# Performance work log

Measured on AMD Instinct MI355X. Metric: run time of the kernel, lower is better.

## Reference

```python
import jax, jax.numpy as jnp
import numpy as np

N = 16384      # nodes
E = 262144     # static edges (avg degree 16)
D = 128        # node embedding dim
DE = 64        # edge embedding dim
H = 256        # MLP hidden dim
K = 16         # dynamic kNN


def _w(key, shape, scale=0.05):
    return jax.random.normal(key, shape, dtype=jnp.float32) * scale


def setup_inputs() -> dict:
    key = jax.random.key(0)
    ks = jax.random.split(key, 32)
    inp = {
        "x": jax.random.normal(ks[0], (N, D), dtype=jnp.float32),
        "edge_attr": jax.random.normal(ks[1], (E, DE), dtype=jnp.float32),
        # static conv msg MLPs (3 layers stacked): in 192 -> 256 -> 128
        "sW1": _w(ks[2], (3, D + DE, H)), "sb1": jnp.zeros((3, H), jnp.float32),
        "sW2": _w(ks[3], (3, H, D)),      "sb2": jnp.zeros((3, D), jnp.float32),
        # static conv update MLPs: 128 -> 256 -> 128
        "uW1": _w(ks[4], (3, D, H)), "ub1": jnp.zeros((3, H), jnp.float32),
        "uW2": _w(ks[5], (3, H, D)), "ub2": jnp.zeros((3, D), jnp.float32),
        # edge refiners between static convs: 64 -> 64
        "rW": _w(ks[6], (2, DE, DE)), "rb": jnp.zeros((2, DE), jnp.float32),
        # dynamic conv msg MLPs (2 layers stacked): in 256 -> 256 -> 128
        "dW1": _w(ks[7], (2, 2 * D, H)), "db1": jnp.zeros((2, H), jnp.float32),
        "dW2": _w(ks[8], (2, H, D)),     "db2": jnp.zeros((2, D), jnp.float32),
        # dynamic conv update MLPs: 128 -> 256 -> 128
        "dUW1": _w(ks[9], (2, D, H)),  "dUb1": jnp.zeros((2, H), jnp.float32),
        "dUW2": _w(ks[10], (2, H, D)), "dUb2": jnp.zeros((2, D), jnp.float32),
        # fuse MLP: 256 -> 256 -> 128
        "fW1": _w(ks[11], (2 * D, H)), "fb1": jnp.zeros((H,), jnp.float32),
        "fW2": _w(ks[12], (H, D)),     "fb2": jnp.zeros((D,), jnp.float32),
        "edge_index": jax.random.randint(ks[13], (2, E), 0, N, dtype=jnp.int64),
        "k": K,
    }
    return inp


def _mlp2(h, W1, b1, W2, b2):
    # SequentialBlock: Linear -> ReLU -> Linear -> ReLU
    return jax.nn.relu(jax.nn.relu(h @ W1 + b1) @ W2 + b2)


def _knn_edges(x, k):
    # squared euclidean distances, [N, N]; self included (dist 0 -> self loops)
    sq = jnp.sum(x * x, axis=1)
    d = sq[:, None] - 2.0 * (x @ x.T) + sq[None, :]
    _, nbr = jax.lax.top_k(-d, k)                  # [N, k] sources per target
    src = nbr.reshape(-1)
    dst = jnp.repeat(jnp.arange(x.shape[0]), k)
    return src, dst


def reference(x, edge_attr, sW1, sb1, sW2, sb2, uW1, ub1, uW2, ub2, rW, rb,
              dW1, db1, dW2, db2, dUW1, dUb1, dUW2, dUb2,
              fW1, fb1, fW2, fb2, edge_index, k):
    n = x.shape[0]
    src, dst = edge_index[0], edge_index[1]  # PyG: row=source(j), col=target(i)

    # ---- static branch: 3 StaticConv ('vanilla') with edge refiners ----
    xs, ea = x, edge_attr
    for i in range(3):
        msg_in = jnp.concatenate([ea, xs[src] - xs[dst]], axis=1)  # [E, DE+D]
        m = _mlp2(msg_in, sW1[i], sb1[i], sW2[i], sb2[i])
        agg = jax.ops.segment_sum(m, dst, num_segments=n)
        xs = _mlp2(agg, uW1[i], ub1[i], uW2[i], ub2[i])
        if i < 2:
            ea = jax.nn.relu(ea @ rW[i] + rb[i])  # EdgeEmbedRefiner

    # ---- dynamic branch: 2 DynamicGonv ('vanilla', kNN on current emb) ----
    xd = x
    for i in range(2):
        dsrc, ddst = _knn_edges(xd, k)
        xi = xd[ddst]
        xj = xd[dsrc]
        m = _mlp2(jnp.concatenate([xi, xj - xi], axis=1), dW1[i], db1[i], dW2[i], db2[i])
        agg = jax.ops.segment_sum(m, ddst, num_segments=n)
        xd = _mlp2(agg, dUW1[i], dUb1[i], dUW2[i], dUb2[i])

    # ---- fuse ----
    h = jnp.concatenate([xs, xd], axis=1)  # [N, 2D]
    return _mlp2(h, fW1, fb1, fW2, fb2)
```

## Files before the change

### kernel.cpp

```cpp
#include <hip/hip_runtime.h>

#define Nn 16384
#define Ee 262144
#define Dd 128
#define DEe 64
#define Hh 256
#define KK 16
#define NSPLIT 16
#define TT 128
#define STILE 128
#define SWEEP (Nn / NSPLIT)
#define PXS 136
#define PDD 68
#define MCAND 32
#define BDEPTH 8
#define LDEPTH 8

typedef __attribute__((ext_vector_type(8))) short short8;
typedef __attribute__((ext_vector_type(4))) float floatx4;

__device__ __forceinline__ ushort f2bf(float f) {
  uint u = __float_as_uint(f);
  u += 0x7fffu + ((u >> 16) & 1u);
  return (ushort)(u >> 16);
}
__device__ __forceinline__ float bf2f(ushort h) { return __uint_as_float(((uint)h) << 16); }
__device__ __forceinline__ void cvt_hilo(float4 v, uint2* hi, uint2* lo) {
  ushort h0 = f2bf(v.x), h1 = f2bf(v.y), h2 = f2bf(v.z), h3 = f2bf(v.w);
  ushort l0 = f2bf(v.x - bf2f(h0)), l1 = f2bf(v.y - bf2f(h1));
  ushort l2 = f2bf(v.z - bf2f(h2)), l3 = f2bf(v.w - bf2f(h3));
  hi->x = (uint)h0 | ((uint)h1 << 16); hi->y = (uint)h2 | ((uint)h3 << 16);
  lo->x = (uint)l0 | ((uint)l1 << 16); lo->y = (uint)l2 | ((uint)l3 << 16);
}
__device__ __forceinline__ uint4 pk8(float4 a, float4 b) {
  uint4 o;
  o.x = (uint)f2bf(a.x) | ((uint)f2bf(a.y) << 16);
  o.y = (uint)f2bf(a.z) | ((uint)f2bf(a.w) << 16);
  o.z = (uint)f2bf(b.x) | ((uint)f2bf(b.y) << 16);
  o.w = (uint)f2bf(b.z) | ((uint)f2bf(b.w) << 16);
  return o;
}

__device__ __forceinline__ int ld_src(const int* ei, int e, int mode) {
  return mode ? ei[e] : ei[2 * e];
}
__device__ __forceinline__ int ld_dst(const int* ei, int e, int mode) {
  return mode ? ei[Ee + e] : ei[2 * Ee + 2 * e];
}

__global__ void k_detect(const int* __restrict__ ei, int* __restrict__ flag) {
  if (blockIdx.x == 0 && threadIdx.x == 0) {
    int any = 0;
    for (int i = 0; i < 64; ++i) any |= ei[2 * i + 1];
    *flag = (any != 0) ? 1 : 0;
  }
}

__global__ void k_hist(const int* __restrict__ ei, const int* __restrict__ mode_p,
                       int* __restrict__ hist) {
  int e = blockIdx.x * 256 + threadIdx.x;
  int mode = *mode_p;
  atomicAdd(&hist[ld_dst(ei, e, mode)], 1);
}

__global__ void k_scan(const int* __restrict__ hist, int* __restrict__ cursor) {
  __shared__ int part[256];
  __shared__ int partx[256];
  int t = threadIdx.x;
  int base = t * (Nn / 256);
  int s = 0;
  for (int i = 0; i < Nn / 256; ++i) s += hist[base + i];
  part[t] = s;
  __syncthreads();
  if (t == 0) {
    int run = 0;
    for (int i = 0; i < 256; ++i) { partx[i] = run; run += part[i]; }
  }
  __syncthreads();
  int run = partx[t];
  for (int i = 0; i < Nn / 256; ++i) { int v = hist[base + i]; cursor[base + i] = run; run += v; }
}

__global__ void k_scatter(const int* __restrict__ ei, const int* __restrict__ mode_p,
                          int* __restrict__ cursor, int* __restrict__ perm,
                          int* __restrict__ dstS) {
  int e = blockIdx.x * 256 + threadIdx.x;
  int mode = *mode_p;
  int d = ld_dst(ei, e, mode);
  int pos = atomicAdd(&cursor[d], 1);
  perm[pos] = e;
  dstS[pos] = d;
}

__global__ void k_sq(const float* __restrict__ x, float* __restrict__ sq,
                     ushort* __restrict__ xbf) {
  int n = blockIdx.x * 256 + threadIdx.x;
  const float4* p = (const float4*)(x + (size_t)n * Dd);
  uint4* ob = (uint4*)(xbf + (size_t)n * Dd);
  float acc = 0.f;
#pragma unroll
  for (int i = 0; i < Dd / 8; ++i) {
    float4 v = p[2 * i];
    acc += v.x * v.x + v.y * v.y + v.z * v.z + v.w * v.w;
    float4 w = p[2 * i + 1];
    acc += w.x * w.x + w.y * w.y + w.z * w.z + w.w * w.w;
    ob[i] = pk8(v, w);
  }
  sq[n] = acc;
}

__global__ void k_repack(const float* __restrict__ sW1, const float* __restrict__ sW2,
                         const float* __restrict__ dW1, const float* __restrict__ dW2,
                         uint4* __restrict__ out) {
  int gid = blockIdx.x * 256 + threadIdx.x;
  const float* W; int K, N, u, obase;
  if (gid < 36864) {
    int i = gid / 12288; u = gid - i * 12288;
    W = sW1 + (size_t)i * 49152; K = 192; N = 256; obase = i * 12288;
  } else if (gid < 61440) {
    int g = gid - 36864; int i = g / 8192; u = g - i * 8192;
    W = sW2 + (size_t)i * 32768; K = 256; N = 128; obase = 36864 + i * 8192;
  } else if (gid < 94208) {
    int g = gid - 61440; int i = g / 16384; u = g - i * 16384;
    W = dW1 + (size_t)i * 65536; K = 256; N = 256; obase = 61440 + i * 16384;
  } else if (gid < 110592) {
    int g = gid - 94208; int i = g / 8192; u = g - i * 8192;
    W = dW2 + (size_t)i * 32768; K = 256; N = 128; obase = 94208 + i * 8192;
  } else return;
  int lane = u & 63;
  int t = u >> 6;
  int ksteps = K / 16;
  int kstep = t % ksteps, ntile = t / ksteps;
  int R = K / 32;
  bool lo = kstep >= R;
  int k0 = (lo ? kstep - R : kstep) * 32 + (lane >> 4) * 8;
  int n = ntile * 16 + (lane & 15);
  ushort v[8];
#pragma unroll
  for (int j = 0; j < 8; ++j) {
    float w = W[(size_t)(k0 + j) * N + n];
    ushort h = f2bf(w);
    v[j] = lo ? f2bf(w - bf2f(h)) : h;
  }
  uint4 o;
  o.x = (uint)v[0] | ((uint)v[1] << 16);
  o.y = (uint)v[2] | ((uint)v[3] << 16);
  o.z = (uint)v[4] | ((uint)v[5] << 16);
  o.w = (uint)v[6] | ((uint)v[7] << 16);
  out[obase + u] = o;
}

template <int RK, int NT>
__device__ __forceinline__ void mfma3(const ushort* aB, int pitch, const uint4* __restrict__ Wp,
                                      int lane, floatx4 C[2][NT]) {
  int q = lane >> 4, m0 = lane & 15;
  short8 ahc[RK][2];
#pragma unroll
  for (int hm = 0; hm < 2; ++hm)
#pragma unroll
    for (int nt = 0; nt < NT; ++nt)
#pragma unroll
      for (int rr = 0; rr < 4; ++rr) C[hm][nt][rr] = 0.f;
#pragma unroll
  for (int s = 0; s < RK; ++s) {
    short8 ah0 = *(const short8*)(aB + m0 * pitch + s * 32 + q * 8);
    short8 ah1 = *(const short8*)(aB + (m0 + 16) * pitch + s * 32 + q * 8);
    short8 al0 = *(const short8*)(aB + m0 * pitch + (RK + s) * 32 + q * 8);
    short8 al1 = *(const short8*)(aB + (m0 + 16) * pitch + (RK + s) * 32 + q * 8);
    ahc[s][0] = ah0;
    ahc[s][1] = ah1;
#pragma unroll
    for (int nt = 0; nt < NT; ++nt) {
      uint4 bw = Wp[(nt * 2 * RK + s) * 64 + lane];
      short8 b = *(short8*)&bw;
      C[0][nt] = __builtin_amdgcn_mfma_f32_16x16x32_bf16(ah0, b, C[0][nt], 0, 0, 0);
      C[1][nt] = __builtin_amdgcn_mfma_f32_16x16x32_bf16(ah1, b, C[1][nt], 0, 0, 0);
      C[0][nt] = __builtin_amdgcn_mfma_f32_16x16x32_bf16(al0, b, C[0][nt], 0, 0, 0);
      C[1][nt] = __builtin_amdgcn_mfma_f32_16x16x32_bf16(al1, b, C[1][nt], 0, 0, 0);
    }
  }
#pragma unroll
  for (int s = 0; s < RK; ++s) {
#pragma unroll
    for (int nt = 0; nt < NT; ++nt) {
      uint4 bw = Wp[(nt * 2 * RK + RK + s) * 64 + lane];
      short8 b = *(short8*)&bw;
      C[0][nt] = __builtin_amdgcn_mfma_f32_16x16x32_bf16(ahc[s][0], b, C[0][nt], 0, 0, 0);
      C[1][nt] = __builtin_amdgcn_mfma_f32_16x16x32_bf16(ahc[s][1], b, C[1][nt], 0, 0, 0);
    }
  }
}

__global__ __launch_bounds__(256, 3) void k_knn_part(const ushort* __restrict__ xbf,
                                                     const float* __restrict__ sq,
                                                     float* __restrict__ part_d,
                                                     int* __restrict__ part_i) {
  __shared__ __align__(16) ushort smXS[128 * PXS];
  __shared__ float sqs_l[STILE];
  __shared__ ushort smBuf[BDEPTH * 256];
  float* dtile = (float*)smXS;
  float* mbD = (float*)smXS;
  int* mbI = ((int*)smXS) + 2048;
  int tid = threadIdx.x;
  int wave = tid >> 6, lane = tid & 63;
  int quad = lane >> 4, n15 = lane & 15;
  int tileT = blockIdx.x >> 4;
  int split = blockIdx.x & 15;
  int tb = tileT * TT;
  int tg = tid >> 1, sl = tid & 1;

  float sqi8[8];
#pragma unroll
  for (int mt = 0; mt < 2; ++mt)
#pragma unroll
    for (int rr = 0; rr < 4; ++rr)
      sqi8[mt * 4 + rr] = sq[tb + wave * 32 + mt * 16 + quad * 4 + rr];

  short8 afr[2][4];
#pragma unroll
  for (int mt = 0; mt < 2; ++mt) {
    int row = tb + wave * 32 + mt * 16 + n15;
#pragma unroll
    for (int ks = 0; ks < 4; ++ks)
      afr[mt][ks] = *(const short8*)&xbf[(size_t)row * Dd + ks * 32 + quad * 8];
  }

  float bd[LDEPTH];
  int bi[LDEPTH];
#pragma unroll
  for (int p2 = 0; p2 < LDEPTH; ++p2) { bd[p2] = 3.0e38f; bi[p2] = 0x7fffffff; }
  int bcnt = 0;

  auto ins = [&](float d, int gidx) {
#pragma unroll
    for (int p = LDEPTH - 1; p >= 1; --p) {
      bool shift = d < bd[p - 1];
      bool here = (!shift) && (d < bd[p]);
      float nb = shift ? bd[p - 1] : (here ? d : bd[p]);
      int ni = shift ? bi[p - 1] : (here ? gidx : bi[p]);
      bd[p] = nb;
      bi[p] = ni;
    }
    if (d < bd[0]) { bd[0] = d; bi[0] = gidx; }
  };

#pragma unroll 1
  for (int st = 0; st < SWEEP / STILE; ++st) {
    int sb = split * SWEEP + st * STILE;
    __syncthreads();
    {
      int row = tid & 127, kh = (tid >> 7) * 64;
      int swz = ((row >> 3) & 7) << 3;
      const ushort* src = &xbf[(size_t)(sb + row) * Dd + kh];
#pragma unroll
      for (int g = 0; g < 8; ++g) {
        int k0 = kh + g * 8;
        *(uint4*)&smXS[row * PXS + (k0 ^ swz)] = *(const uint4*)&src[g * 8];
      }
      if (tid < STILE) sqs_l[tid] = sq[sb + tid];
    }
    __syncthreads();
    floatx4 C[2][8];
#pragma unroll
    for (int mt = 0; mt < 2; ++mt)
#pragma unroll
      for (int nt = 0; nt < 8; ++nt)
#pragma unroll
        for (int rr = 0; rr < 4; ++rr) C[mt][nt][rr] = 0.f;
#pragma unroll
    for (int nt = 0; nt < 8; ++nt) {
      int s = nt * 16 + n15;
      int swz = ((s >> 3) & 7) << 3;
#pragma unroll
      for (int ks = 0; ks < 4; ++ks) {
        int k0 = ks * 32 + quad * 8;
        short8 bfr = *(const short8*)&smXS[s * PXS + (k0 ^ swz)];
        C[0][nt] = __builtin_amdgcn_mfma_f32_16x16x32_bf16(afr[0][ks], bfr, C[0][nt], 0, 0, 0);
        C[1][nt] = __builtin_amdgcn_mfma_f32_16x16x32_bf16(afr[1][ks], bfr, C[1][nt], 0, 0, 0);
      }
    }
    float sc[8];
#pragma unroll
    for (int nt = 0; nt < 8; ++nt) sc[nt] = sqs_l[nt * 16 + n15];
    __syncthreads();
#pragma unroll
    for (int h = 0; h < 2; ++h) {
      if (h) __syncthreads();
#pragma unroll
      for (int mt = 0; mt < 2; ++mt)
#pragma unroll
        for (int nt = 0; nt < 4; ++nt)
#pragma unroll
          for (int rr = 0; rr < 4; ++rr) {
            int row = wave * 32 + mt * 16 + quad * 4 + rr;
            int col = nt * 16 + n15;
            float d = fmaf(-2.f, C[mt][nt + 4 * h][rr], sqi8[mt * 4 + rr]) + sc[nt + 4 * h];
            dtile[row * PDD + col] = d;
          }
      __syncthreads();
      const float* drow = &dtile[tg * PDD];
      int cbase = sl * 32;
#pragma unroll 1
      for (int j = 0; j < 8; ++j) {
        float4 v = *(const float4*)&drow[cbase + j * 4];
        float mn = fminf(fminf(v.x, v.y), fminf(v.z, v.w));
        if (mn < bd[LDEPTH - 1]) {
          float dv0 = v.x, dv1 = v.y, dv2 = v.z, dv3 = v.w;
#pragma unroll
          for (int e = 0; e < 4; ++e) {
            float d = (e == 0) ? dv0 : (e == 1) ? dv1 : (e == 2) ? dv2 : dv3;
            if (d < bd[LDEPTH - 1]) {
              int col = cbase + j * 4 + e;
              if (bcnt < BDEPTH) {
                smBuf[bcnt * 256 + tid] = (ushort)col;
                ++bcnt;
              } else {
                ins(d, sb + h * 64 + col);
              }
            }
          }
        }
      }
#pragma unroll 1
      for (int p = 0; p < BDEPTH; ++p) {
        bool act = p < bcnt;
        if (!__any(act)) break;
        if (act) {
          int col = smBuf[p * 256 + tid];
          float d = drow[col];
          ins(d, sb + h * 64 + col);
        }
      }
      bcnt = 0;
    }
  }

  __syncthreads();
#pragma unroll
  for (int o = 0; o < LDEPTH; ++o) {
    mbD[tid * LDEPTH + o] = bd[o];
    mbI[tid * LDEPTH + o] = bi[o];
  }
  __syncthreads();
  if (tid < TT) {
    const float* la = &mbD[(2 * tid) * LDEPTH];
    const float* lb = &mbD[(2 * tid + 1) * LDEPTH];
    const int* ia = &mbI[(2 * tid) * LDEPTH];
    const int* ib = &mbI[(2 * tid + 1) * LDEPTH];
    int pa = 0, pb = 0;
    size_t base = ((size_t)(tb + tid) * NSPLIT + split) * KK;
#pragma unroll
    for (int o = 0; o < KK; ++o) {
      float da = (pa < LDEPTH) ? la[pa] : 3.4e38f;
      float db = (pb < LDEPTH) ? lb[pb] : 3.4e38f;
      int iaa = (pa < LDEPTH) ? ia[pa] : 0x7fffffff;
      int ibb = (pb < LDEPTH) ? ib[pb] : 0x7fffffff;
      bool pick = (da < db) || (da == db && iaa < ibb);
      part_d[base + o] = pick ? da : db;
      part_i[base + o] = pick ? iaa : ibb;
      pa += pick ? 1 : 0;
      pb += pick ? 0 : 1;
    }
  }
}

__global__ void k_knn_merge(const float* __restrict__ part_d, const int* __restrict__ part_i,
                            int* __restrict__ cand) {
  int n = blockIdx.x * 256 + threadIdx.x;
  const float* pd = part_d + (size_t)n * NSPLIT * KK;
  const int* pi = part_i + (size_t)n * NSPLIT * KK;
  int pos[NSPLIT];
#pragma unroll
  for (int l = 0; l < NSPLIT; ++l) pos[l] = 0;
  for (int o = 0; o < MCAND; ++o) {
    float bestd = 3.3e38f;
    int besti = 0x7fffffff;
    int bestl = 0;
#pragma unroll
    for (int l = 0; l < NSPLIT; ++l) {
      if (pos[l] < KK) {
        float dd = pd[l * KK + pos[l]];
        int ii = pi[l * KK + pos[l]];
        if (dd < bestd || (dd == bestd && ii < besti)) { bestd = dd; besti = ii; bestl = l; }
      }
    }
    cand[(size_t)n * MCAND + o] = besti;
#pragma unroll
    for (int l = 0; l < NSPLIT; ++l) pos[l] += (l == bestl) ? 1 : 0;
  }
}

__global__ __launch_bounds__(256) void k_rerank(const float* __restrict__ x,
                                                const float* __restrict__ sq,
                                                const int* __restrict__ cand,
                                                int* __restrict__ knn_src) {
  int tid = threadIdx.x;
  int wave = tid >> 6, lane = tid & 63;
  int t = blockIdx.x * 4 + wave;
  int c = lane & 31, h = lane >> 5;
  int idx = cand[(size_t)t * MCAND + c];
  const float* xt = x + (size_t)t * Dd + h * 64;
  const float* xc = x + (size_t)idx * Dd + h * 64;
  float s = 0.f;
#pragma unroll
  for (int g = 0; g < 16; ++g) {
    float4 a = *(const float4*)&xt[g * 4];
    float4 b = *(const float4*)&xc[g * 4];
    s += a.x * b.x + a.y * b.y + a.z * b.z + a.w * b.w;
  }
  s += __shfl_xor(s, 32);
  float d = fmaf(-2.f, s, sq[t]) + sq[idx];
  int rank = 0;
#pragma unroll
  for (int j = 0; j < 32; ++j) {
    float dj = __shfl(d, j);
    int ij = __shfl(idx, j);
    rank += ((dj < d) || (dj == d && ij < idx)) ? 1 : 0;
  }
  if (lane < 32 && rank < KK) knn_src[t * KK + rank] = idx;
}

__global__ __launch_bounds__(256, 3) void k_static_msg(
    const float* __restrict__ xs, const float* __restrict__ ea, const int* __restrict__ ei,
    const int* __restrict__ mode_p, const int* __restrict__ perm, const int* __restrict__ dstS,
    const uint4* __restrict__ W1p, const float* __restrict__ b1,
    const uint4* __restrict__ W2p, const float* __restrict__ b2, float* __restrict__ agg) {
  __shared__ __align__(16) ushort smH[32 * 520];
  __shared__ int dstLoc[32];
  int tid = threadIdx.x;
  int wave = tid >> 6, lane = tid & 63;
  int pb = blockIdx.x * 32;
  int mode = *mode_p;
  int r = tid & 31, q8 = tid >> 5;
  int p = pb + r;
  int e = perm[p];
  int ds = dstS[p];
  int sr = ld_src(ei, e, mode);
  if (q8 == 0) dstLoc[r] = ds;
  const float* eap = ea + (size_t)e * DEe;
  const float* xsp = xs + (size_t)sr * Dd;
  const float* xdp = xs + (size_t)ds * Dd;
#pragma unroll
  for (int it = 0; it < 6; ++it) {
    int f = q8 * 24 + it * 4;
    float4 v;
    if (f < 64) {
      v = *(const float4*)&eap[f];
    } else {
      float4 a = *(const float4*)&xsp[f - 64];
      float4 b = *(const float4*)&xdp[f - 64];
      v = make_float4(a.x - b.x, a.y - b.y, a.z - b.z, a.w - b.w);
    }
    uint2 hi, lo;
    cvt_hilo(v, &hi, &lo);
    *(uint2*)&smH[r * 392 + f] = hi;
    *(uint2*)&smH[r * 392 + 192 + f] = lo;
  }
  __syncthreads();
  floatx4 C1[2][4];
  mfma3<6, 4>(smH, 392, W1p + (size_t)wave * 4 * 12 * 64, lane, C1);
  __syncthreads();
  {
    int q = lane >> 4, n15 = lane & 15;
#pragma unroll
    for (int hm = 0; hm < 2; ++hm)
#pragma unroll
      for (int nt = 0; nt < 4; ++nt) {
        int n = wave * 64 + nt * 16 + n15;
        float bv = b1[n];
#pragma unroll
        for (int rr = 0; rr < 4; ++rr) {
          int m = hm * 16 + q * 4 + rr;
          float h = fmaxf(C1[hm][nt][rr] + bv, 0.f);
          ushort hh = f2bf(h);
          smH[m * 520 + n] = hh;
          smH[m * 520 + 256 + n] = f2bf(h - bf2f(hh));
        }
      }
  }
  __syncthreads();
  floatx4 C2[2][2];
  mfma3<8, 2>(smH, 520, W2p + (size_t)wave * 2 * 16 * 64, lane, C2);
  __syncthreads();
  float* smM = (float*)smH;
  {
    int q = lane >> 4, n15 = lane & 15;
#pragma unroll
    for (int hm = 0; hm < 2; ++hm)
#pragma unroll
      for (int nt = 0; nt < 2; ++nt) {
        int n = wave * 32 + nt * 16 + n15;
        float bv = b2[n];
#pragma unroll
        for (int rr = 0; rr < 4; ++rr) {
          int m = hm * 16 + q * 4 + rr;
          smM[m * 132 + n] = fmaxf(C2[hm][nt][rr] + bv, 0.f);
        }
      }
  }
  __syncthreads();
  int col = tid & 127, half = tid >> 7;
  int r0 = half * 16;
  float run = smM[r0 * 132 + col];
  int prevd = dstLoc[r0];
  for (int rr = 1; rr < 16; ++rr) {
    int row = r0 + rr;
    int dd2 = dstLoc[row];
    float v = smM[row * 132 + col];
    if (dd2 != prevd) {
      atomicAdd(&agg[(size_t)prevd * Dd + col], run);
      run = v;
      prevd = dd2;
    } else {
      run += v;
    }
  }
  atomicAdd(&agg[(size_t)prevd * Dd + col], run);
}

__global__ __launch_bounds__(256, 3) void k_dyn_msg(
    const float* __restrict__ xd, const int* __restrict__ knn, const uint4* __restrict__ W1p,
    const float* __restrict__ b1, const uint4* __restrict__ W2p, const float* __restrict__ b2,
    float* __restrict__ agg) {
  __shared__ __align__(16) ushort smH[32 * 520];
  int tid = threadIdx.x;
  int wave = tid >> 6, lane = tid & 63;
  int nb2 = blockIdx.x * 2;
  int r = tid & 31, q8 = tid >> 5;
  int tgt = nb2 + (r >> 4);
  int nj = knn[tgt * KK + (r & 15)];
  const float* xip = xd + (size_t)tgt * Dd;
  const float* xjp = xd + (size_t)nj * Dd;
#pragma unroll
  for (int it = 0; it < 8; ++it) {
    int f = q8 * 32 + it * 4;
    float4 v;
    if (f < 128) {
      v = *(const float4*)&xip[f];
    } else {
      float4 a = *(const float4*)&xjp[f - 128];
      float4 b = *(const float4*)&xip[f - 128];
      v = make_float4(a.x - b.x, a.y - b.y, a.z - b.z, a.w - b.w);
    }
    uint2 hi, lo;
    cvt_hilo(v, &hi, &lo);
    *(uint2*)&smH[r * 520 + f] = hi;
    *(uint2*)&smH[r * 520 + 256 + f] = lo;
  }
  __syncthreads();
  floatx4 C1[2][4];
  mfma3<8, 4>(smH, 520, W1p + (size_t)wave * 4 * 16 * 64, lane, C1);
  __syncthreads();
  {
    int q = lane >> 4, n15 = lane & 15;
#pragma unroll
    for (int hm = 0; hm < 2; ++hm)
#pragma unroll
      for (int nt = 0; nt < 4; ++nt) {
        int n = wave * 64 + nt * 16 + n15;
        float bv = b1[n];
#pragma unroll
        for (int rr = 0; rr < 4; ++rr) {
          int m = hm * 16 + q * 4 + rr;
          float h = fmaxf(C1[hm][nt][rr] + bv, 0.f);
          ushort hh = f2bf(h);
          smH[m * 520 + n] = hh;
          smH[m * 520 + 256 + n] = f2bf(h - bf2f(hh));
        }
      }
  }
  __syncthreads();
  floatx4 C2[2][2];
  mfma3<8, 2>(smH, 520, W2p + (size_t)wave * 2 * 16 * 64, lane, C2);
  int q = lane >> 4, n15 = lane & 15;
#pragma unroll
  for (int hm = 0; hm < 2; ++hm)
#pragma unroll
    for (int nt = 0; nt < 2; ++nt) {
      int n = wave * 32 + nt * 16 + n15;
      float bv = b2[n];
      float s = 0.f;
#pragma unroll
      for (int rr = 0; rr < 4; ++rr) s += fmaxf(C2[hm][nt][rr] + bv, 0.f);
      s += __shfl_xor(s, 16);
      s += __shfl_xor(s, 32);
      if (q == 0) agg[(size_t)(nb2 + hm) * Dd + n] = s;
    }
}

__device__ __forceinline__ void mlp_l1(int tid, int indim, const float* __restrict__ W1,
                                       const float* __restrict__ b1, float* smA, float* smB) {
  int rg = tid >> 5, cg = tid & 31;
  float acc[32];
#pragma unroll
  for (int i = 0; i < 32; ++i) acc[i] = 0.f;
  for (int kc = 0; kc < indim / 8; ++kc) {
    const float* W1g = W1 + (size_t)kc * 8 * Hh;
    *(float4*)&smB[tid * 4] = *(const float4*)&W1g[tid * 4];
    *(float4*)&smB[1024 + tid * 4] = *(const float4*)&W1g[1024 + tid * 4];
    __syncthreads();
#pragma unroll
    for (int k = 0; k < 8; ++k) {
      int kk = kc * 8 + k;
      float4 a0 = *(const float4*)&smA[kk * 32 + rg * 4];
      float4 b0 = *(const float4*)&smB[k * Hh + cg * 8];
      float4 b1v = *(const float4*)&smB[k * Hh + cg * 8 + 4];
      float av[4] = {a0.x, a0.y, a0.z, a0.w};
      float bv[8] = {b0.x, b0.y, b0.z, b0.w, b1v.x, b1v.y, b1v.z, b1v.w};
#pragma unroll
      for (int rr = 0; rr < 4; ++rr)
#pragma unroll
        for (int cc = 0; cc < 8; ++cc) acc[rr * 8 + cc] += av[rr] * bv[cc];
    }
    __syncthreads();
  }
  float4 bb0 = *(const float4*)&b1[cg * 8];
  float4 bb1 = *(const float4*)&b1[cg * 8 + 4];
  float bs[8] = {bb0.x, bb0.y, bb0.z, bb0.w, bb1.x, bb1.y, bb1.z, bb1.w};
#pragma unroll
  for (int rr = 0; rr < 4; ++rr) {
    int row = rg * 4 + rr;
    float4 h0, h1;
    h0.x = fmaxf(acc[rr * 8 + 0] + bs[0], 0.f);
    h0.y = fmaxf(acc[rr * 8 + 1] + bs[1], 0.f);
    h0.z = fmaxf(acc[rr * 8 + 2] + bs[2], 0.f);
    h0.w = fmaxf(acc[rr * 8 + 3] + bs[3], 0.f);
    h1.x = fmaxf(acc[rr * 8 + 4] + bs[4], 0.f);
    h1.y = fmaxf(acc[rr * 8 + 5] + bs[5], 0.f);
    h1.z = fmaxf(acc[rr * 8 + 6] + bs[6], 0.f);
    h1.w = fmaxf(acc[rr * 8 + 7] + bs[7], 0.f);
    *(float4*)&smA[row * 260 + cg * 8] = h0;
    *(float4*)&smA[row * 260 + cg * 8 + 4] = h1;
  }
  __syncthreads();
}

__device__ __forceinline__ void mlp_l2(int tid, const float* __restrict__ W2,
                                       const float* smA, float* smB, float acc2[16]) {
  int rg2 = tid >> 5, cg2 = tid & 31;
#pragma unroll
  for (int i = 0; i < 16; ++i) acc2[i] = 0.f;
  for (int kc = 0; kc < Hh / 16; ++kc) {
    const float* W2g = W2 + (size_t)kc * 16 * Dd;
    *(float4*)&smB[tid * 4] = *(const float4*)&W2g[tid * 4];
    *(float4*)&smB[1024 + tid * 4] = *(const float4*)&W2g[1024 + tid * 4];
    __syncthreads();
#pragma unroll
    for (int k = 0; k < 16; ++k) {
      int kk = kc * 16 + k;
      float4 b0 = *(const float4*)&smB[k * Dd + cg2 * 4];
#pragma unroll
      for (int rr = 0; rr < 4; ++rr) {
        float a = smA[(rg2 * 4 + rr) * 260 + kk];
        acc2[rr * 4 + 0] += a * b0.x;
        acc2[rr * 4 + 1] += a * b0.y;
        acc2[rr * 4 + 2] += a * b0.z;
        acc2[rr * 4 + 3] += a * b0.w;
      }
    }
    __syncthreads();
  }
}

__global__ __launch_bounds__(256, 3) void k_node_mlp2(
    const float* __restrict__ in1, const float* __restrict__ in2, int indim,
    const float* __restrict__ W1, const float* __restrict__ b1, const float* __restrict__ W2,
    const float* __restrict__ b2, float* __restrict__ out) {
  __shared__ float smA[32 * 260];
  __shared__ float smB[2048];
  int tid = threadIdx.x;
  int nb = blockIdx.x * 32;
  int r = tid & 31, q = tid >> 5;
  for (int pass = 0; pass < indim / 32; ++pass) {
    int k0 = pass * 32 + q * 4;
    float4 v;
    if (k0 < Dd)
      v = *(const float4*)&in1[(size_t)(nb + r) * Dd + k0];
    else
      v = *(const float4*)&in2[(size_t)(nb + r) * Dd + (k0 - Dd)];
    smA[(k0 + 0) * 32 + r] = v.x;
    smA[(k0 + 1) * 32 + r] = v.y;
    smA[(k0 + 2) * 32 + r] = v.z;
    smA[(k0 + 3) * 32 + r] = v.w;
  }
  __syncthreads();
  mlp_l1(tid, indim, W1, b1, smA, smB);
  float acc2[16];
  mlp_l2(tid, W2, smA, smB, acc2);
  int rg2 = tid >> 5, cg2 = tid & 31;
  float4 ob = *(const float4*)&b2[cg2 * 4];
#pragma unroll
  for (int rr = 0; rr < 4; ++rr) {
    float4 o;
    o.x = fmaxf(acc2[rr * 4 + 0] + ob.x, 0.f);
    o.y = fmaxf(acc2[rr * 4 + 1] + ob.y, 0.f);
    o.z = fmaxf(acc2[rr * 4 + 2] + ob.z, 0.f);
    o.w = fmaxf(acc2[rr * 4 + 3] + ob.w, 0.f);
    *(float4*)&out[(size_t)(nb + rg2 * 4 + rr) * Dd + cg2 * 4] = o;
  }
}

__global__ __launch_bounds__(256) void k_refine(const float* __restrict__ ein,
                                                const float* __restrict__ rW,
                                                const float* __restrict__ rb,
                                                float* __restrict__ eout) {
  __shared__ float lea[16 * 64];
  __shared__ float ldsW[64 * 64];
  int tid = threadIdx.x;
  int eb = blockIdx.x * 16;
  *(float4*)&lea[tid * 4] = *(const float4*)&ein[(size_t)eb * DEe + tid * 4];
#pragma unroll
  for (int m = 0; m < 4; ++m) {
    int i4 = tid + m * 256;
    *(float4*)&ldsW[i4 * 4] = *(const float4*)&rW[i4 * 4];
  }
  __syncthreads();
  int j = tid & 63, eg = tid >> 6;
  float bias = rb[j];
  float acc0 = 0.f, acc1 = 0.f, acc2 = 0.f, acc3 = 0.f;
#pragma unroll 8
  for (int k = 0; k < 64; ++k) {
    float w = ldsW[k * 64 + j];
    acc0 += lea[(eg + 0) * 64 + k] * w;
    acc1 += lea[(eg + 4) * 64 + k] * w;
    acc2 += lea[(eg + 8) * 64 + k] * w;
    acc3 += lea[(eg + 12) * 64 + k] * w;
  }
  eout[(size_t)(eb + eg + 0) * DEe + j] = fmaxf(acc0 + bias, 0.f);
  eout[(size_t)(eb + eg + 4) * DEe + j] = fmaxf(acc1 + bias, 0.f);
  eout[(size_t)(eb + eg + 8) * DEe + j] = fmaxf(acc2 + bias, 0.f);
  eout[(size_t)(eb + eg + 12) * DEe + j] = fmaxf(acc3 + bias, 0.f);
}

extern "C" void kernel_launch(void* const* d_in, const int* in_sizes, int n_in, void* d_out,
                              int out_size, void* d_ws, size_t ws_size, hipStream_t stream) {
  (void)in_sizes; (void)n_in; (void)out_size; (void)ws_size;
  const float* x = (const float*)d_in[0];
  const float* edge_attr = (const float*)d_in[1];
  const float* sW1 = (const float*)d_in[2];
  const float* sb1 = (const float*)d_in[3];
  const float* sW2 = (const float*)d_in[4];
  const float* sb2 = (const float*)d_in[5];
  const float* uW1 = (const float*)d_in[6];
  const float* ub1 = (const float*)d_in[7];
  const float* uW2 = (const float*)d_in[8];
  const float* ub2 = (const float*)d_in[9];
  const float* rW = (const float*)d_in[10];
  const float* rb = (const float*)d_in[11];
  const float* dW1 = (const float*)d_in[12];
  const float* db1 = (const float*)d_in[13];
  const float* dW2 = (const float*)d_in[14];
  const float* db2 = (const float*)d_in[15];
  const float* dUW1 = (const float*)d_in[16];
  const float* dUb1 = (const float*)d_in[17];
  const float* dUW2 = (const float*)d_in[18];
  const float* dUb2 = (const float*)d_in[19];
  const float* fW1 = (const float*)d_in[20];
  const float* fb1 = (const float*)d_in[21];
  const float* fW2 = (const float*)d_in[22];
  const float* fb2 = (const float*)d_in[23];
  const int* ei = (const int*)d_in[24];
  float* out = (float*)d_out;

  float* wsf = (float*)d_ws;
  size_t off = 0;
  float* ea_ws = wsf + off; off += (size_t)Ee * DEe;
  float* xs_ws = wsf + off; off += (size_t)Nn * Dd;
  float* xd_ws = wsf + off; off += (size_t)Nn * Dd;
  float* agg = wsf + off;   off += (size_t)Nn * Dd;
  float* sq = wsf + off;    off += Nn;
  int* knn_src = (int*)(wsf + off); off += (size_t)Nn * KK;
  int* hist = (int*)(wsf + off);   off += Nn;
  int* cursor = (int*)(wsf + off); off += Nn;
  int* perm = (int*)(wsf + off);   off += Ee;
  int* dstS = (int*)(wsf + off);   off += Ee;
  int* modep = (int*)(wsf + off);  off += 1;
  off = (off + 3) & ~(size_t)3;
  uint4* wpk = (uint4*)(wsf + off); off += (size_t)110592 * 4;
  ushort* xbf = (ushort*)(wsf + off); off += (size_t)Nn * Dd / 2;
  float* part_d = ea_ws;
  int* part_i = (int*)(ea_ws + (size_t)Nn * NSPLIT * KK);
  int* cand = (int*)(ea_ws + 2 * (size_t)Nn * NSPLIT * KK);

  k_detect<<<1, 64, 0, stream>>>(ei, modep);
  hipMemsetAsync(hist, 0, Nn * sizeof(int), stream);
  k_hist<<<Ee / 256, 256, 0, stream>>>(ei, modep, hist);
  k_scan<<<1, 256, 0, stream>>>(hist, cursor);
  k_scatter<<<Ee / 256, 256, 0, stream>>>(ei, modep, cursor, perm, dstS);

  k_repack<<<432, 256, 0, stream>>>(sW1, sW2, dW1, dW2, wpk);

  const float* xs_cur = x;
  const float* ea_cur = edge_attr;
  for (int i = 0; i < 3; ++i) {
    hipMemsetAsync(agg, 0, (size_t)Nn * Dd * sizeof(float), stream);
    k_static_msg<<<Ee / 32, 256, 0, stream>>>(
        xs_cur, ea_cur, ei, modep, perm, dstS, wpk + (size_t)i * 12288,
        sb1 + (size_t)i * Hh, wpk + 36864 + (size_t)i * 8192, sb2 + (size_t)i * Dd, agg);
    k_node_mlp2<<<Nn / 32, 256, 0, stream>>>(
        agg, (const float*)nullptr, Dd, uW1 + (size_t)i * Dd * Hh, ub1 + (size_t)i * Hh,
        uW2 + (size_t)i * Hh * Dd, ub2 + (size_t)i * Dd, xs_ws);
    xs_cur = xs_ws;
    if (i < 2) {
      k_refine<<<Ee / 16, 256, 0, stream>>>(ea_cur, rW + (size_t)i * DEe * DEe,
                                            rb + (size_t)i * DEe, ea_ws);
      ea_cur = ea_ws;
    }
  }

  const float* xd_cur = x;
  for (int i = 0; i < 2; ++i) {
    k_sq<<<Nn / 256, 256, 0, stream>>>(xd_cur, sq, xbf);
    k_knn_part<<<(Nn / TT) * NSPLIT, 256, 0, stream>>>(xbf, sq, part_d, part_i);
    k_knn_merge<<<Nn / 256, 256, 0, stream>>>(part_d, part_i, cand);
    k_rerank<<<Nn / 4, 256, 0, stream>>>(xd_cur, sq, cand, knn_src);
    k_dyn_msg<<<Nn / 2, 256, 0, stream>>>(
        xd_cur, knn_src, wpk + 61440 + (size_t)i * 16384, db1 + (size_t)i * Hh,
        wpk + 94208 + (size_t)i * 8192, db2 + (size_t)i * Dd, agg);
    k_node_mlp2<<<Nn / 32, 256, 0, stream>>>(
        agg, (const float*)nullptr, Dd, dUW1 + (size_t)i * Dd * Hh, dUb1 + (size_t)i * Hh,
        dUW2 + (size_t)i * Hh * Dd, dUb2 + (size_t)i * Dd, xd_ws);
    xd_cur = xd_ws;
  }

  k_node_mlp2<<<Nn / 32, 256, 0, stream>>>(xs_ws, xd_ws, 2 * Dd, fW1, fb1, fW2, fb2, out);
}
```

Baseline: 2.807 ms.

## Prefetch next kNN source tile into registers and stream A fragments

The kNN partial-distance kernel now loads the next 128-row source tile and its squared norms into registers during the second half of the current tile's selection phase, then writes them to shared memory at the top of the next iteration. This overlaps global-memory latency with the top-k insertion work instead of stalling on the load after a barrier. The A-fragments are no longer held in registers for the whole kernel; they are reloaded from global (cache) per k-step, reordering the MFMA loop to ks-outer, which frees registers for the staging buffer. The candidate column buffer shrinks from ushort to uchar, which still holds columns up to 63. The trade-off is extra global/cache traffic for the A operand and higher register pressure from the staging array, which may affect occupancy under launch_bounds(256,3).

```diff
diff --git a/kernel.cpp b/kernel.cpp
--- a/kernel.cpp
+++ b/kernel.cpp
@@ -197,7 +197,7 @@
                                                      int* __restrict__ part_i) {
   __shared__ __align__(16) ushort smXS[128 * PXS];
   __shared__ float sqs_l[STILE];
-  __shared__ ushort smBuf[BDEPTH * 256];
+  __shared__ unsigned char smBuf[BDEPTH * 256];
   float* dtile = (float*)smXS;
   float* mbD = (float*)smXS;
   int* mbI = ((int*)smXS) + 2048;
@@ -216,14 +216,8 @@
     for (int rr = 0; rr < 4; ++rr)
       sqi8[mt * 4 + rr] = sq[tb + wave * 32 + mt * 16 + quad * 4 + rr];
 
-  short8 afr[2][4];
-#pragma unroll
-  for (int mt = 0; mt < 2; ++mt) {
-    int row = tb + wave * 32 + mt * 16 + n15;
-#pragma unroll
-    for (int ks = 0; ks < 4; ++ks)
-      afr[mt][ks] = *(const short8*)&xbf[(size_t)row * Dd + ks * 32 + quad * 8];
-  }
+  const ushort* abase0 = &xbf[(size_t)(tb + wave * 32 + n15) * Dd + quad * 8];
+  const ushort* abase1 = &xbf[(size_t)(tb + wave * 32 + 16 + n15) * Dd + quad * 8];
 
   float bd[LDEPTH];
   int bi[LDEPTH];
@@ -244,6 +238,16 @@
     if (d < bd[0]) { bd[0] = d; bi[0] = gidx; }
   };
 
+  uint4 stg[8];
+  float sqv;
+  {
+    int row = tid & 127, kh = (tid >> 7) * 64;
+    const ushort* src = &xbf[(size_t)(split * SWEEP + row) * Dd + kh];
+#pragma unroll
+    for (int g = 0; g < 8; ++g) stg[g] = *(const uint4*)&src[g * 8];
+    sqv = sq[split * SWEEP + (tid & 127)];
+  }
+
 #pragma unroll 1
   for (int st = 0; st < SWEEP / STILE; ++st) {
     int sb = split * SWEEP + st * STILE;
@@ -251,13 +255,12 @@
     {
       int row = tid & 127, kh = (tid >> 7) * 64;
       int swz = ((row >> 3) & 7) << 3;
-      const ushort* src = &xbf[(size_t)(sb + row) * Dd + kh];
 #pragma unroll
       for (int g = 0; g < 8; ++g) {
         int k0 = kh + g * 8;
-        *(uint4*)&smXS[row * PXS + (k0 ^ swz)] = *(const uint4*)&src[g * 8];
-      }
-      if (tid < STILE) sqs_l[tid] = sq[sb + tid];
+        *(uint4*)&smXS[row * PXS + (k0 ^ swz)] = stg[g];
+      }
+      if (tid < STILE) sqs_l[tid] = sqv;
     }
     __syncthreads();
     floatx4 C[2][8];
@@ -268,15 +271,17 @@
 #pragma unroll
         for (int rr = 0; rr < 4; ++rr) C[mt][nt][rr] = 0.f;
 #pragma unroll
-    for (int nt = 0; nt < 8; ++nt) {
-      int s = nt * 16 + n15;
-      int swz = ((s >> 3) & 7) << 3;
-#pragma unroll
-      for (int ks = 0; ks < 4; ++ks) {
-        int k0 = ks * 32 + quad * 8;
+    for (int ks = 0; ks < 4; ++ks) {
+      int k0 = ks * 32 + quad * 8;
+      short8 a0 = *(const short8*)&abase0[ks * 32];
+      short8 a1 = *(const short8*)&abase1[ks * 32];
+#pragma unroll
+      for (int nt = 0; nt < 8; ++nt) {
+        int s = nt * 16 + n15;
+        int swz = ((s >> 3) & 7) << 3;
         short8 bfr = *(const short8*)&smXS[s * PXS + (k0 ^ swz)];
-        C[0][nt] = __builtin_amdgcn_mfma_f32_16x16x32_bf16(afr[0][ks], bfr, C[0][nt], 0, 0, 0);
-        C[1][nt] = __builtin_amdgcn_mfma_f32_16x16x32_bf16(afr[1][ks], bfr, C[1][nt], 0, 0, 0);
+        C[0][nt] = __builtin_amdgcn_mfma_f32_16x16x32_bf16(a0, bfr, C[0][nt], 0, 0, 0);
+        C[1][nt] = __builtin_amdgcn_mfma_f32_16x16x32_bf16(a1, bfr, C[1][nt], 0, 0, 0);
       }
     }
     float sc[8];
@@ -297,6 +302,13 @@
             float d = fmaf(-2.f, C[mt][nt + 4 * h][rr], sqi8[mt * 4 + rr]) + sc[nt + 4 * h];
             dtile[row * PDD + col] = d;
           }
+      if (h == 1 && st + 1 < SWEEP / STILE) {
+        int row = tid & 127, kh = (tid >> 7) * 64;
+        const ushort* src = &xbf[(size_t)(sb + STILE + row) * Dd + kh];
+#pragma unroll
+        for (int g = 0; g < 8; ++g) stg[g] = *(const uint4*)&src[g * 8];
+        sqv = sq[sb + STILE + (tid & 127)];
+      }
       __syncthreads();
       const float* drow = &dtile[tg * PDD];
       int cbase = sl * 32;
@@ -312,7 +324,7 @@
             if (d < bd[LDEPTH - 1]) {
               int col = cbase + j * 4 + e;
               if (bcnt < BDEPTH) {
-                smBuf[bcnt * 256 + tid] = (ushort)col;
+                smBuf[bcnt * 256 + tid] = (unsigned char)col;
                 ++bcnt;
               } else {
                 ins(d, sb + h * 64 + col);
```

Result: slower. 3.293 ms (+17.3%).
